# Performance work log

Measured on AMD Instinct MI355X. Metric: run time of the kernel, lower is better.

The kernel has to match this reference:

```python
import jax, jax.numpy as jnp
import numpy as np

N_OUT, N_IN, K = 64, 64, 3


def setup_inputs() -> dict:
    key = jax.random.key(0)
    ks = jax.random.split(key, 6)
    bs, emb_dim, g_latent = 32, 512, 256
    w_flat = N_OUT * N_IN * K * K  # 36864
    return {
        "emb": jax.random.normal(ks[0], (bs, emb_dim), jnp.float32),
        "x": jax.random.normal(ks[1], (bs, N_IN, 96, 96), jnp.float32),
        "w1_w": jax.random.normal(ks[2], (g_latent, emb_dim), jnp.float32) * (1.0 / np.sqrt(emb_dim)),
        "w1_b": jax.random.normal(ks[3], (g_latent,), jnp.float32) * 0.01,
        "w2_w": jax.random.normal(ks[4], (w_flat, g_latent), jnp.float32) * (1.0 / np.sqrt(g_latent)),
        "w2_b": jax.random.normal(ks[5], (w_flat,), jnp.float32) * 0.01,
    }


def reference(emb, x, w1_w, w1_b, w2_w, w2_b):
    bs, c, h, w = x.shape
    # Hypernetwork: Linear -> ReLU -> Linear, predicting per-sample conv weights
    hdn = jax.nn.relu(emb @ w1_w.T + w1_b)                      # [bs, g_latent]
    weights = (hdn @ w2_w.T + w2_b).reshape(bs * N_OUT, N_IN, K, K)
    # Per-sample conv via grouped conv trick: x -> (1, bs*c, h, w), groups=bs
    xtag = x.reshape(1, bs * c, h, w)
    out = jax.lax.conv_general_dilated(
        xtag, weights,
        window_strides=(1, 1), padding=((0, 0), (0, 0)),
        dimension_numbers=("NCHW", "OIHW", "NCHW"),
        feature_group_count=bs,
    )  # [1, bs*N_OUT, h-K+1, w-K+1]
    return out.reshape(bs, N_OUT, out.shape[-2], out.shape[-1])
```

## Files before the change

kernel.cpp:

```cpp
#include <hip/hip_runtime.h>

typedef __attribute__((ext_vector_type(8)))  _Float16 half8;
typedef __attribute__((ext_vector_type(4)))  _Float16 half4;
typedef __attribute__((ext_vector_type(16))) float    f32x16;

#define G_LATENT 256
#define EMB      512
#define WFLAT    36864

__global__ __launch_bounds__(256) void k1_hdn(
    const float* __restrict__ emb, const float* __restrict__ w1w,
    const float* __restrict__ w1b, float* __restrict__ hdn)
{
    const int s = blockIdx.x;
    const int j = threadIdx.x;
    const float4* e4 = (const float4*)(emb + (size_t)s * EMB);
    const float4* w4 = (const float4*)(w1w + (size_t)j * EMB);
    float acc = 0.f;
#pragma unroll 8
    for (int k = 0; k < EMB / 4; ++k) {
        float4 a = e4[k], b = w4[k];
        acc += a.x * b.x + a.y * b.y + a.z * b.z + a.w * b.w;
    }
    acc += w1b[j];
    hdn[s * G_LATENT + j] = fmaxf(acc, 0.f);
}

__global__ __launch_bounds__(256) void k2_wfrag(
    const float* __restrict__ hdn, const float* __restrict__ w2w,
    const float* __restrict__ w2b, _Float16* __restrict__ wfrag)
{
    const int tid  = threadIdx.x;
    const int lane = tid & 63;
    const int h    = lane >> 5, n31 = lane & 31;
    const int rtile = blockIdx.x * 4 + (tid >> 6);
    const int r     = rtile * 32 + n31;

    half8 afr[16];
#pragma unroll
    for (int kb = 0; kb < 16; ++kb) {
        const float* p = hdn + n31 * G_LATENT + kb * 16 + 4 * h;
        float4 q0 = *(const float4*)p;
        float4 q1 = *(const float4*)(p + 8);
        half8 a;
        a[0] = (_Float16)q0.x; a[1] = (_Float16)q0.y;
        a[2] = (_Float16)q0.z; a[3] = (_Float16)q0.w;
        a[4] = (_Float16)q1.x; a[5] = (_Float16)q1.y;
        a[6] = (_Float16)q1.z; a[7] = (_Float16)q1.w;
        afr[kb] = a;
    }

    f32x16 acc = {0,0,0,0,0,0,0,0,0,0,0,0,0,0,0,0};
    const float* wrow = w2w + (size_t)r * G_LATENT;
#pragma unroll
    for (int kb = 0; kb < 16; ++kb) {
        float4 q0 = *(const float4*)(wrow + kb * 16 + 4 * h);
        float4 q1 = *(const float4*)(wrow + kb * 16 + 4 * h + 8);
        half8 bfr;
        bfr[0] = (_Float16)q0.x; bfr[1] = (_Float16)q0.y;
        bfr[2] = (_Float16)q0.z; bfr[3] = (_Float16)q0.w;
        bfr[4] = (_Float16)q1.x; bfr[5] = (_Float16)q1.y;
        bfr[6] = (_Float16)q1.z; bfr[7] = (_Float16)q1.w;
        acc = __builtin_amdgcn_mfma_f32_32x32x16_f16(afr[kb], bfr, acc, 0, 0, 0);
    }

    const float bias = w2b[r];
    const int oc  = r / 576;
    const int rem = r - oc * 576;
    const int ic  = rem / 9;
    const int khw = rem - ic * 9;
    const int octile = oc >> 5, l31 = oc & 31;
    const int kb4 = ic >> 4, i16 = ic & 15;
    const int hh  = (i16 >> 2) & 1;
    const int e   = (i16 & 3) + 4 * (i16 >> 3);
    const int lanep = l31 + 32 * hh;
#pragma unroll
    for (int g = 0; g < 16; ++g) {
        const int srow = (g & 3) + 8 * (g >> 2) + 4 * h;
        const size_t idx =
            (((((size_t)srow * 9 + khw) * 4 + kb4) * 2 + octile) * 64 + lanep) * 8 + e;
        wfrag[idx] = (_Float16)(acc[g] + bias);
    }
}

#define TRO  12
#define XRN  14
#define XCN  34
#define NSPX (XRN * XCN)

__global__ __launch_bounds__(256, 2) void k3_conv(
    const float* __restrict__ x, const _Float16* __restrict__ wfrag,
    float* __restrict__ out)
{
    __shared__ __align__(16) unsigned char lds[NSPX * 128];

    const int b  = blockIdx.x;
    const int wg = (b & 7) * 96 + (b >> 3);
    const int ct = wg % 3;
    const int rt = (wg / 3) & 7;
    const int s  = wg / 24;
    const int rbase = rt * TRO, cbase = ct * 32;
    const int tid = threadIdx.x;

    for (int i = tid; i < 30 * 256; i += 256) {
        const int spx = (i & 15) + ((i >> 8) << 4);
        if (spx < NSPX) {
            const int q  = (i >> 4) & 15;
            const int xr = spx / XCN;
            const int xc = spx - xr * XCN;
            const int gr = rbase + xr, gc = cbase + xc;
            float f0 = 0.f, f1 = 0.f, f2 = 0.f, f3 = 0.f;
            if (gr < 96 && gc < 96) {
                const float* px = x + (size_t)(s * 64 + q * 4) * 9216 + gr * 96 + gc;
                f0 = px[0];
                f1 = px[9216];
                f2 = px[2 * 9216];
                f3 = px[3 * 9216];
            }
            half4 hv;
            hv[0] = (_Float16)f0; hv[1] = (_Float16)f1;
            hv[2] = (_Float16)f2; hv[3] = (_Float16)f3;
            const int qoff = ((q >> 2) << 5) + ((q & 1) << 4) + (((q >> 1) & 1) << 3);
            const int addr = ((spx << 7) + qoff) ^ ((spx & 7) << 4);
            *(half4*)(lds + addr) = hv;
        }
    }
    __syncthreads();

    const int lane = tid & 63, wv = tid >> 6;
    const int h = lane >> 5, n31 = lane & 31;

    const f32x16 z16 = {0,0,0,0,0,0,0,0,0,0,0,0,0,0,0,0};
    f32x16 acc[2][3];
#pragma unroll
    for (int o = 0; o < 2; ++o)
#pragma unroll
        for (int n = 0; n < 3; ++n) acc[o][n] = z16;

    const half8* __restrict__ A = (const half8*)(wfrag + (size_t)s * WFLAT);

    for (int khw = 0; khw < 9; ++khw) {
        const int kh = khw / 3;
        const int kw = khw - kh * 3;
        const int rowb = (wv * 3 + kh) * XCN + n31 + kw;
#pragma unroll
        for (int kb = 0; kb < 4; ++kb) {
            const half8 a0 = A[((khw * 4 + kb) * 2 + 0) * 64 + lane];
            const half8 a1 = A[((khw * 4 + kb) * 2 + 1) * 64 + lane];
#pragma unroll
            for (int n = 0; n < 3; ++n) {
                const int spx  = rowb + n * XCN;
                const int addr = ((spx << 7) + (kb << 5) + (h << 4)) ^ ((spx & 7) << 4);
                const half8 bb = *(const half8*)(lds + addr);
                acc[0][n] = __builtin_amdgcn_mfma_f32_32x32x16_f16(a0, bb, acc[0][n], 0, 0, 0);
                acc[1][n] = __builtin_amdgcn_mfma_f32_32x32x16_f16(a1, bb, acc[1][n], 0, 0, 0);
            }
        }
    }

    const int ocol = cbase + n31;
    if (ocol < 94) {
#pragma unroll
        for (int ot = 0; ot < 2; ++ot) {
#pragma unroll
            for (int n = 0; n < 3; ++n) {
                const int orow = rbase + wv * 3 + n;
                if (orow < 94) {
                    float* po = out + (size_t)(s * 64 + ot * 32 + 4 * h) * 8836
                                    + orow * 94 + ocol;
#pragma unroll
                    for (int g = 0; g < 16; ++g) {
                        const int od = (g & 3) + 8 * (g >> 2);
                        po[(size_t)od * 8836] = acc[ot][n][g];
                    }
                }
            }
        }
    }
}

extern "C" void kernel_launch(void* const* d_in, const int* in_sizes, int n_in,
                              void* d_out, int out_size, void* d_ws, size_t ws_size,
                              hipStream_t stream)
{
    (void)in_sizes; (void)n_in; (void)out_size; (void)ws_size;
    const float* emb = (const float*)d_in[0];
    const float* x   = (const float*)d_in[1];
    const float* w1w = (const float*)d_in[2];
    const float* w1b = (const float*)d_in[3];
    const float* w2w = (const float*)d_in[4];
    const float* w2b = (const float*)d_in[5];
    float* out = (float*)d_out;

    float*    hdn   = (float*)d_ws;
    _Float16* wfrag = (_Float16*)((char*)d_ws + 32 * 1024);

    k1_hdn<<<32, 256, 0, stream>>>(emb, w1w, w1b, hdn);
    k2_wfrag<<<288, 256, 0, stream>>>(hdn, w2w, w2b, wfrag);
    k3_conv<<<768, 256, 0, stream>>>(x, wfrag, out);
}
```

Measured before the change: 244.3 us.

## Restructure hypernet weight GEMM with LDS staging and vectorize conv input tile loads

k1 now writes the hidden activations directly as pre-swizzled fp16 MFMA fragments. k2 is rebuilt so each block owns a (khw, kb, octile, ihalf) slice: it double-buffers coalesced w2 row loads through LDS and stages its output in LDS before writing contiguous half4 chunks. This replaces the former scattered 2-byte stores. k3 loads x with float4 reads into a new channel-fragment LDS layout and shifts the edge tiles to overlap rather than pad, which removes the bounds checks and zero-fill. Together these cut uncoalesced global traffic in the weight-generation and input-staging phases, at the cost of more complex indexing and extra synchronisation.

Result: faster. 227.0 us (-7.1%).

```diff
diff --git a/kernel.cpp b/kernel.cpp
--- a/kernel.cpp
+++ b/kernel.cpp
@@ -10,119 +10,157 @@
 
 __global__ __launch_bounds__(256) void k1_hdn(
     const float* __restrict__ emb, const float* __restrict__ w1w,
-    const float* __restrict__ w1b, float* __restrict__ hdn)
+    const float* __restrict__ w1b, _Float16* __restrict__ hdn16)
 {
     const int s = blockIdx.x;
     const int j = threadIdx.x;
     const float4* e4 = (const float4*)(emb + (size_t)s * EMB);
     const float4* w4 = (const float4*)(w1w + (size_t)j * EMB);
-    float acc = 0.f;
+    float a0 = 0.f, a1 = 0.f;
 #pragma unroll 8
-    for (int k = 0; k < EMB / 4; ++k) {
-        float4 a = e4[k], b = w4[k];
-        acc += a.x * b.x + a.y * b.y + a.z * b.z + a.w * b.w;
-    }
-    acc += w1b[j];
-    hdn[s * G_LATENT + j] = fmaxf(acc, 0.f);
+    for (int k = 0; k < EMB / 4; k += 2) {
+        float4 a = e4[k],     b = w4[k];
+        float4 c = e4[k + 1], d = w4[k + 1];
+        a0 += a.x * b.x + a.y * b.y + a.z * b.z + a.w * b.w;
+        a1 += c.x * d.x + c.y * d.y + c.z * d.z + c.w * d.w;
+    }
+    const float acc = fmaxf(a0 + a1 + w1b[j], 0.f);
+    const int kb = j >> 4;
+    const int h  = (j >> 2) & 1;
+    const int e  = (j & 3) + 4 * ((j >> 3) & 1);
+    hdn16[(kb * 64 + s + 32 * h) * 8 + e] = (_Float16)acc;
 }
 
 __global__ __launch_bounds__(256) void k2_wfrag(
-    const float* __restrict__ hdn, const float* __restrict__ w2w,
+    const _Float16* __restrict__ hdn16, const float* __restrict__ w2w,
     const float* __restrict__ w2b, _Float16* __restrict__ wfrag)
 {
-    const int tid  = threadIdx.x;
-    const int lane = tid & 63;
-    const int h    = lane >> 5, n31 = lane & 31;
-    const int rtile = blockIdx.x * 4 + (tid >> 6);
-    const int r     = rtile * 32 + n31;
-
-    half8 afr[16];
-#pragma unroll
-    for (int kb = 0; kb < 16; ++kb) {
-        const float* p = hdn + n31 * G_LATENT + kb * 16 + 4 * h;
-        float4 q0 = *(const float4*)p;
-        float4 q1 = *(const float4*)(p + 8);
-        half8 a;
-        a[0] = (_Float16)q0.x; a[1] = (_Float16)q0.y;
-        a[2] = (_Float16)q0.z; a[3] = (_Float16)q0.w;
-        a[4] = (_Float16)q1.x; a[5] = (_Float16)q1.y;
-        a[6] = (_Float16)q1.z; a[7] = (_Float16)q1.w;
-        afr[kb] = a;
-    }
-
-    f32x16 acc = {0,0,0,0,0,0,0,0,0,0,0,0,0,0,0,0};
-    const float* wrow = w2w + (size_t)r * G_LATENT;
-#pragma unroll
-    for (int kb = 0; kb < 16; ++kb) {
-        float4 q0 = *(const float4*)(wrow + kb * 16 + 4 * h);
-        float4 q1 = *(const float4*)(wrow + kb * 16 + 4 * h + 8);
-        half8 bfr;
-        bfr[0] = (_Float16)q0.x; bfr[1] = (_Float16)q0.y;
-        bfr[2] = (_Float16)q0.z; bfr[3] = (_Float16)q0.w;
-        bfr[4] = (_Float16)q1.x; bfr[5] = (_Float16)q1.y;
-        bfr[6] = (_Float16)q1.z; bfr[7] = (_Float16)q1.w;
-        acc = __builtin_amdgcn_mfma_f32_32x32x16_f16(afr[kb], bfr, acc, 0, 0, 0);
-    }
-
-    const float bias = w2b[r];
-    const int oc  = r / 576;
-    const int rem = r - oc * 576;
-    const int ic  = rem / 9;
-    const int khw = rem - ic * 9;
-    const int octile = oc >> 5, l31 = oc & 31;
-    const int kb4 = ic >> 4, i16 = ic & 15;
-    const int hh  = (i16 >> 2) & 1;
-    const int e   = (i16 & 3) + 4 * (i16 >> 3);
-    const int lanep = l31 + 32 * hh;
-#pragma unroll
-    for (int g = 0; g < 16; ++g) {
-        const int srow = (g & 3) + 8 * (g >> 2) + 4 * h;
-        const size_t idx =
-            (((((size_t)srow * 9 + khw) * 4 + kb4) * 2 + octile) * 64 + lanep) * 8 + e;
-        wfrag[idx] = (_Float16)(acc[g] + bias);
-    }
-}
-
-#define TRO  12
-#define XRN  14
-#define XCN  34
-#define NSPX (XRN * XCN)
+    __shared__ __align__(16) _Float16 sm[8 * 256 * 8];
+
+    const int b     = blockIdx.x;
+    const int ihalf = b & 1;
+    const int oct   = (b >> 1) & 1;
+    const int kbc   = (b >> 2) & 3;
+    const int khw   = b >> 4;
+
+    const int t = threadIdx.x, lane = t & 63, wv = t >> 6;
+    const int h = lane >> 5, l31 = lane & 31;
+
+    const int oc31 = t & 31, icof = t >> 5;
+    const size_t rrow = (size_t)(oct * 32 + oc31) * 576
+                      + (size_t)(kbc * 16 + ihalf * 8 + icof) * 9 + khw;
+    const float* wrow = w2w + rrow * G_LATENT;
+
+    float bias[2];
+#pragma unroll
+    for (int ntl = 0; ntl < 2; ++ntl) {
+        const int nt = wv * 2 + ntl;
+        const size_t rc = (size_t)(oct * 32 + l31) * 576
+                        + (size_t)(kbc * 16 + ihalf * 8 + nt) * 9 + khw;
+        bias[ntl] = w2b[rc];
+    }
+
+    const f32x16 z16 = {0,0,0,0,0,0,0,0,0,0,0,0,0,0,0,0};
+    f32x16 acc[2] = {z16, z16};
+
+    float4 ld[2][16];
+#pragma unroll
+    for (int u = 0; u < 16; ++u) ld[0][u] = ((const float4*)wrow)[u];
+
+    const half8* __restrict__ hfr = (const half8*)hdn16;
+
+#pragma unroll
+    for (int kc = 0; kc < 4; ++kc) {
+        __syncthreads();
+        if (kc < 3) {
+            const float4* nxt = (const float4*)(wrow + (kc + 1) * 64);
+#pragma unroll
+            for (int u = 0; u < 16; ++u) ld[(kc + 1) & 1][u] = nxt[u];
+        }
+#pragma unroll
+        for (int kb16 = 0; kb16 < 4; ++kb16) {
+#pragma unroll
+            for (int hh = 0; hh < 2; ++hh) {
+                const float4 lo = ld[kc & 1][kb16 * 4 + hh];
+                const float4 hi = ld[kc & 1][kb16 * 4 + 2 + hh];
+                half8 c;
+                c[0] = (_Float16)lo.x; c[1] = (_Float16)lo.y;
+                c[2] = (_Float16)lo.z; c[3] = (_Float16)lo.w;
+                c[4] = (_Float16)hi.x; c[5] = (_Float16)hi.y;
+                c[6] = (_Float16)hi.z; c[7] = (_Float16)hi.w;
+                *(half8*)&sm[((kb16 * 2 + hh) * 256 + t) * 8] = c;
+            }
+        }
+        __syncthreads();
+#pragma unroll
+        for (int kb16 = 0; kb16 < 4; ++kb16) {
+            const half8 af = hfr[(kc * 4 + kb16) * 64 + lane];
+#pragma unroll
+            for (int ntl = 0; ntl < 2; ++ntl) {
+                const int lr = (wv * 2 + ntl) * 32 + l31;
+                const half8 bf = *(const half8*)&sm[((kb16 * 2 + h) * 256 + lr) * 8];
+                acc[ntl] = __builtin_amdgcn_mfma_f32_32x32x16_f16(af, bf, acc[ntl], 0, 0, 0);
+            }
+        }
+    }
+
+    __syncthreads();
+#pragma unroll
+    for (int ntl = 0; ntl < 2; ++ntl) {
+        const int nt    = wv * 2 + ntl;
+        const int lanep = l31 + 32 * (nt >> 2);
+        const int elow  = nt & 3;
+#pragma unroll
+        for (int g = 0; g < 16; ++g) {
+            const int srow = (g & 3) + 8 * (g >> 2) + 4 * h;
+            sm[(srow * 64 + lanep) * 4 + elow] = (_Float16)(acc[ntl][g] + bias[ntl]);
+        }
+    }
+    __syncthreads();
+#pragma unroll
+    for (int i = 0; i < 8; ++i) {
+        const int c = t + 256 * i;
+        const int s  = c >> 6, lp = c & 63;
+        const half4 hv = *(const half4*)&sm[c * 4];
+        _Float16* dst = wfrag + ((((size_t)s * 9 + khw) * 4 + kbc) * 2 + oct) * 512
+                              + lp * 8 + ihalf * 4;
+        *(half4*)dst = hv;
+    }
+}
 
 __global__ __launch_bounds__(256, 2) void k3_conv(
     const float* __restrict__ x, const _Float16* __restrict__ wfrag,
     float* __restrict__ out)
 {
-    __shared__ __align__(16) unsigned char lds[NSPX * 128];
+    __shared__ __align__(16) _Float16 lds[14 * 8 * 36 * 8];
 
     const int b  = blockIdx.x;
     const int wg = (b & 7) * 96 + (b >> 3);
     const int ct = wg % 3;
     const int rt = (wg / 3) & 7;
     const int s  = wg / 24;
-    const int rbase = rt * TRO, cbase = ct * 32;
+    const int rbase  = (rt < 7) ? rt * 12 : 82;
+    const int wstart = (ct == 0) ? 0 : (ct == 1) ? 32 : 60;
+    const int dlt    = (ct == 2) ? 2 : 0;
     const int tid = threadIdx.x;
 
-    for (int i = tid; i < 30 * 256; i += 256) {
-        const int spx = (i & 15) + ((i >> 8) << 4);
-        if (spx < NSPX) {
-            const int q  = (i >> 4) & 15;
-            const int xr = spx / XCN;
-            const int xc = spx - xr * XCN;
-            const int gr = rbase + xr, gc = cbase + xc;
-            float f0 = 0.f, f1 = 0.f, f2 = 0.f, f3 = 0.f;
-            if (gr < 96 && gc < 96) {
-                const float* px = x + (size_t)(s * 64 + q * 4) * 9216 + gr * 96 + gc;
-                f0 = px[0];
-                f1 = px[9216];
-                f2 = px[2 * 9216];
-                f3 = px[3 * 9216];
-            }
-            half4 hv;
-            hv[0] = (_Float16)f0; hv[1] = (_Float16)f1;
-            hv[2] = (_Float16)f2; hv[3] = (_Float16)f3;
-            const int qoff = ((q >> 2) << 5) + ((q & 1) << 4) + (((q >> 1) & 1) << 3);
-            const int addr = ((spx << 7) + qoff) ^ ((spx & 7) << 4);
-            *(half4*)(lds + addr) = hv;
+    if (tid < 252) {
+        const int p9 = tid % 9, q9 = tid / 9;
+        const float* xs = x + (size_t)s * 64 * 9216 + (size_t)rbase * 96
+                            + wstart + p9 * 4;
+#pragma unroll 4
+        for (int i = 0; i < 32; ++i) {
+            const int piece = q9 + 28 * i;
+            const int xr = piece >> 6, ch = piece & 63;
+            const float4 v = *(const float4*)(xs + (size_t)ch * 9216 + xr * 96);
+            const int kb = ch >> 4, c16 = ch & 15;
+            const int hh = (c16 >> 2) & 1;
+            const int pz = (c16 & 3) + 4 * ((c16 >> 3) & 1);
+            const int base = ((xr * 8 + kb * 2 + hh) * 36 + p9 * 4) * 8 + pz;
+            lds[base]      = (_Float16)v.x;
+            lds[base + 8]  = (_Float16)v.y;
+            lds[base + 16] = (_Float16)v.z;
+            lds[base + 24] = (_Float16)v.w;
         }
     }
     __syncthreads();
@@ -139,41 +177,38 @@
 
     const half8* __restrict__ A = (const half8*)(wfrag + (size_t)s * WFLAT);
 
-    for (int khw = 0; khw < 9; ++khw) {
-        const int kh = khw / 3;
-        const int kw = khw - kh * 3;
-        const int rowb = (wv * 3 + kh) * XCN + n31 + kw;
-#pragma unroll
-        for (int kb = 0; kb < 4; ++kb) {
-            const half8 a0 = A[((khw * 4 + kb) * 2 + 0) * 64 + lane];
-            const half8 a1 = A[((khw * 4 + kb) * 2 + 1) * 64 + lane];
-#pragma unroll
-            for (int n = 0; n < 3; ++n) {
-                const int spx  = rowb + n * XCN;
-                const int addr = ((spx << 7) + (kb << 5) + (h << 4)) ^ ((spx & 7) << 4);
-                const half8 bb = *(const half8*)(lds + addr);
-                acc[0][n] = __builtin_amdgcn_mfma_f32_32x32x16_f16(a0, bb, acc[0][n], 0, 0, 0);
-                acc[1][n] = __builtin_amdgcn_mfma_f32_32x32x16_f16(a1, bb, acc[1][n], 0, 0, 0);
-            }
-        }
-    }
-
-    const int ocol = cbase + n31;
-    if (ocol < 94) {
-#pragma unroll
-        for (int ot = 0; ot < 2; ++ot) {
-#pragma unroll
-            for (int n = 0; n < 3; ++n) {
-                const int orow = rbase + wv * 3 + n;
-                if (orow < 94) {
-                    float* po = out + (size_t)(s * 64 + ot * 32 + 4 * h) * 8836
-                                    + orow * 94 + ocol;
-#pragma unroll
-                    for (int g = 0; g < 16; ++g) {
-                        const int od = (g & 3) + 8 * (g >> 2);
-                        po[(size_t)od * 8836] = acc[ot][n][g];
-                    }
+    for (int kh = 0; kh < 3; ++kh) {
+        for (int kw = 0; kw < 3; ++kw) {
+            const int khw = kh * 3 + kw;
+            const int xc  = dlt + n31 + kw;
+#pragma unroll
+            for (int kb = 0; kb < 4; ++kb) {
+                const half8 a0 = A[((khw * 4 + kb) * 2 + 0) * 64 + lane];
+                const half8 a1 = A[((khw * 4 + kb) * 2 + 1) * 64 + lane];
+#pragma unroll
+                for (int n = 0; n < 3; ++n) {
+                    const int xr = wv * 3 + n + kh;
+                    const half8 bb =
+                        *(const half8*)&lds[((xr * 8 + kb * 2 + h) * 36 + xc) * 8];
+                    acc[0][n] = __builtin_amdgcn_mfma_f32_32x32x16_f16(a0, bb, acc[0][n], 0, 0, 0);
+                    acc[1][n] = __builtin_amdgcn_mfma_f32_32x32x16_f16(a1, bb, acc[1][n], 0, 0, 0);
                 }
+            }
+        }
+    }
+
+    const int ocol = wstart + dlt + n31;
+#pragma unroll
+    for (int ot = 0; ot < 2; ++ot) {
+#pragma unroll
+        for (int n = 0; n < 3; ++n) {
+            const int orow = rbase + wv * 3 + n;
+            float* po = out + (size_t)(s * 64 + ot * 32 + 4 * h) * 8836
+                            + orow * 94 + ocol;
+#pragma unroll
+            for (int g = 0; g < 16; ++g) {
+                const int od = (g & 3) + 8 * (g >> 2);
+                po[(size_t)od * 8836] = acc[ot][n][g];
             }
         }
     }
@@ -192,10 +227,10 @@
     const float* w2b = (const float*)d_in[5];
     float* out = (float*)d_out;
 
-    float*    hdn   = (float*)d_ws;
+    _Float16* hdn16 = (_Float16*)d_ws;
     _Float16* wfrag = (_Float16*)((char*)d_ws + 32 * 1024);
 
-    k1_hdn<<<32, 256, 0, stream>>>(emb, w1w, w1b, hdn);
-    k2_wfrag<<<288, 256, 0, stream>>>(hdn, w2w, w2b, wfrag);
+    k1_hdn<<<32, 256, 0, stream>>>(emb, w1w, w1b, hdn16);
+    k2_wfrag<<<144, 256, 0, stream>>>(hdn16, w2w, w2b, wfrag);
     k3_conv<<<768, 256, 0, stream>>>(x, wfrag, out);
 }
```
